# Optimization experiments

Measured on AMD Instinct MI355X. Metric: run time of the kernel, lower is better.

The kernel has to match this reference:

```python
import jax, jax.numpy as jnp
import numpy as np

S, B, HID, NH = 256, 2, 512, 8
HD = HID // NH
C = 1.0            # Poincare ball curvature c (geoopt k = -c)
SQC = C ** 0.5
EPS = 1e-15


def _artanh(x):
    return jnp.arctanh(jnp.clip(x, -1 + 1e-7, 1 - 1e-7))


def artan_k(x):
    return _artanh(SQC * x) / SQC


def tan_k(x):
    return jnp.tanh(SQC * x) / SQC


def mobius_add(x, y):
    x2 = jnp.sum(x * x, -1, keepdims=True)
    y2 = jnp.sum(y * y, -1, keepdims=True)
    xy = jnp.sum(x * y, -1, keepdims=True)
    num = (1 + 2 * C * xy + C * y2) * x + (1 - C * x2) * y
    den = 1 + 2 * C * xy + C * C * x2 * y2
    return num / jnp.maximum(den, EPS)


def mobius_matvec(W, x):
    x_norm = jnp.maximum(jnp.linalg.norm(x, axis=-1, keepdims=True), EPS)
    mx = x @ W.T
    mx_norm = jnp.maximum(jnp.linalg.norm(mx, axis=-1, keepdims=True), EPS)
    res = tan_k(mx_norm / x_norm * artan_k(x_norm)) * (mx / mx_norm)
    zero = jnp.all(mx == 0, axis=-1, keepdims=True)
    return jnp.where(zero, 0.0, res)


def projx(x):
    n = jnp.maximum(jnp.linalg.norm(x, axis=-1, keepdims=True), EPS)
    maxnorm = (1 - 4e-3) / SQC  # float32 eps in geoopt
    return jnp.where(n > maxnorm, x / n * maxnorm, x)


def expmap0(u):
    n = jnp.maximum(jnp.linalg.norm(u, axis=-1, keepdims=True), EPS)
    return tan_k(n) * u / n


def logmap0(y):
    n = jnp.maximum(jnp.linalg.norm(y, axis=-1, keepdims=True), EPS)
    return artan_k(n) * y / n


def mobius_scalar_mul(r, x):
    n = jnp.maximum(jnp.linalg.norm(x, axis=-1, keepdims=True), EPS)
    return tan_k(r * artan_k(n)) * x / n


def manifold_linear(W, b, x):
    return projx(mobius_add(mobius_matvec(W, x), b))


def setup_inputs() -> dict:
    key = jax.random.key(0)
    ks = jax.random.split(key, 7)
    q = jax.random.normal(ks[0], (S, B, HID), jnp.float32) * 0.02
    w = lambda k: jax.random.normal(k, (HID, HID), jnp.float32) * 0.02
    bias = lambda k: jax.random.normal(k, (HID,), jnp.float32) * 0.01
    return {"query": q,
            "Wq": w(ks[1]), "bq": bias(ks[2]),
            "Wk": w(ks[3]), "bk": bias(ks[4]),
            "Wv": w(ks[5]), "bv": bias(ks[6])}


def reference(query, Wq, bq, Wk, bk, Wv, bv):
    x = jnp.transpose(query, (1, 0, 2))  # [B,S,HID], key=value=query
    Bn, Sn, _ = x.shape
    q = manifold_linear(Wq, bq, x)
    k = manifold_linear(Wk, bk, x)
    v = manifold_linear(Wv, bv, x)
    # faithful to torch .view(-1, H, S, D): plain memory reshape (not transpose)
    ql = expmap0(logmap0(q).reshape(Bn, NH, Sn, HD))
    kl = expmap0(logmap0(k).reshape(Bn, NH, Sn, HD))
    vl = expmap0(logmap0(v).reshape(Bn, NH, Sn, HD))
    # pairwise mobius_add(-q, k) -> [B,H,Q,N,D]; torch norm(p=-2) over D (faithful)
    diff = mobius_add(-ql[:, :, :, None, :], kl[:, :, None, :, :])
    t1 = jnp.sum(jnp.maximum(diff * diff, 1e-30) ** -1.0, axis=-1) ** -0.5
    scores = jnp.clip(-2.0 * artan_k(t1), -1e10, 1e10)
    probs = jax.nn.sigmoid(scores)  # [B,H,Q,N]; dropout p=0 -> identity
    # weighted gyro-midpoint over N (geoopt _weighted_midpoint, reducedim=[-1])
    gamma = 2.0 / jnp.maximum(1.0 - C * jnp.sum(vl * vl, -1), EPS)  # [B,H,N]
    denom = jnp.einsum('bhqn,bhn->bhq', probs, gamma - 1.0)
    sgn = jnp.where(denom >= 0, 1.0, -1.0)
    denom = sgn * jnp.maximum(jnp.abs(denom), 1e-10)
    nom = jnp.einsum('bhqn,bhnd->bhqd', probs, gamma[..., None] * vl)
    ctx = mobius_scalar_mul(0.5, nom / denom[..., None])  # [B,H,Q,D]
    ctx = jnp.transpose(ctx, (0, 2, 1, 3))  # [B,Q,H,D]
    ctx = expmap0(logmap0(ctx).reshape(Bn, Sn, HID))
    return jnp.transpose(ctx, (1, 0, 2)), probs
```

## Files before the change

kernel.cpp:

```cpp
#include <hip/hip_runtime.h>
#include <math.h>

constexpr int S_   = 256;
constexpr int B_   = 2;
constexpr int HID_ = 512;
constexpr int NH_  = 8;
constexpr int HD_  = 64;
constexpr int BSH  = B_ * S_ * HID_;

__device__ __forceinline__ float artanh_c(float x) {
    x = fminf(fmaxf(x, -0.9999999f), 0.9999999f);
    return 0.5f * __logf((1.f + x) / (1.f - x));
}

__device__ __forceinline__ float wsum64(float v) {
    #pragma unroll
    for (int o = 1; o < 64; o <<= 1) v += __shfl_xor(v, o, 64);
    return v;
}

__device__ __forceinline__ float block_sum_256(float v, float* red) {
    const int t = threadIdx.x;
    __syncthreads();
    red[t] = v;
    __syncthreads();
    #pragma unroll
    for (int sft = 128; sft > 0; sft >>= 1) {
        if (t < sft) red[t] += red[t + sft];
        __syncthreads();
    }
    return red[0];
}

constexpr int TM_ = 32, TN_ = 64, KC_ = 32;

__global__ __launch_bounds__(256) void gemm3_kernel(
    const float* __restrict__ query,
    const float* __restrict__ Wq, const float* __restrict__ Wk,
    const float* __restrict__ Wv, float* __restrict__ ws_mx)
{
    const int tid   = threadIdx.x;
    const int which = blockIdx.x >> 7;
    const int tmp   = blockIdx.x & 127;
    const int row0  = (tmp >> 3) * TM_;
    const int col0  = (tmp & 7) * TN_;
    const float* __restrict__ W = (which == 0) ? Wq : (which == 1) ? Wk : Wv;
    float* __restrict__ outp = ws_mx + (size_t)which * (HID_ * HID_);

    __shared__ __align__(16) float sA[KC_][68];
    __shared__ __align__(16) float sB[KC_][68];

    const int sr = tid >> 3;
    const int sk = (tid & 7) * 4;
    const int gra = row0 + sr;
    const float* pa  = query + (size_t)((gra & 255) * 2 + (gra >> 8)) * HID_ + sk;
    const float* pb0 = W + (size_t)(col0 + sr) * HID_ + sk;
    const float* pb1 = W + (size_t)(col0 + sr + 32) * HID_ + sk;

    const int ty = tid >> 4, tx = tid & 15;
    float acc[2][4] = {};

    float4 va  = *(const float4*)pa;
    float4 vb0 = *(const float4*)pb0;
    float4 vb1 = *(const float4*)pb1;
    for (int k0 = 0; k0 < HID_; k0 += KC_) {
        __syncthreads();
        sA[sk+0][sr] = va.x;  sA[sk+1][sr] = va.y;  sA[sk+2][sr] = va.z;  sA[sk+3][sr] = va.w;
        sB[sk+0][sr] = vb0.x; sB[sk+1][sr] = vb0.y; sB[sk+2][sr] = vb0.z; sB[sk+3][sr] = vb0.w;
        sB[sk+0][sr+32] = vb1.x; sB[sk+1][sr+32] = vb1.y; sB[sk+2][sr+32] = vb1.z; sB[sk+3][sr+32] = vb1.w;
        __syncthreads();
        if (k0 + KC_ < HID_) {
            va  = *(const float4*)(pa + k0 + KC_);
            vb0 = *(const float4*)(pb0 + k0 + KC_);
            vb1 = *(const float4*)(pb1 + k0 + KC_);
        }
        #pragma unroll
        for (int kk = 0; kk < KC_; ++kk) {
            const float2 av = *(const float2*)&sA[kk][ty * 2];
            const float4 bv = *(const float4*)&sB[kk][tx * 4];
            acc[0][0] = fmaf(av.x, bv.x, acc[0][0]);
            acc[0][1] = fmaf(av.x, bv.y, acc[0][1]);
            acc[0][2] = fmaf(av.x, bv.z, acc[0][2]);
            acc[0][3] = fmaf(av.x, bv.w, acc[0][3]);
            acc[1][0] = fmaf(av.y, bv.x, acc[1][0]);
            acc[1][1] = fmaf(av.y, bv.y, acc[1][1]);
            acc[1][2] = fmaf(av.y, bv.z, acc[1][2]);
            acc[1][3] = fmaf(av.y, bv.w, acc[1][3]);
        }
    }
    #pragma unroll
    for (int i = 0; i < 2; ++i) {
        float4 o = make_float4(acc[i][0], acc[i][1], acc[i][2], acc[i][3]);
        *(float4*)&outp[(size_t)(row0 + ty * 2 + i) * HID_ + col0 + tx * 4] = o;
    }
}

__global__ __launch_bounds__(256) void mobius_rows_kernel(
    const float* __restrict__ query,
    const float* __restrict__ bq, const float* __restrict__ bk,
    const float* __restrict__ bv,
    float* __restrict__ ws_qkv, float* __restrict__ ws_gamma)
{
    const int lane = threadIdx.x & 63;
    const int wv   = threadIdx.x >> 6;
    const int row  = blockIdx.x * 4 + wv;
    const int which = row >> 9;
    const int rr    = row & 511;
    const float* __restrict__ bias = (which == 0) ? bq : (which == 1) ? bk : bv;
    float* mrow = ws_qkv + (size_t)row * HID_;
    const float* xrow = query + (size_t)((rr & 255) * 2 + (rr >> 8)) * HID_;

    float m[8], x[8], bb[8];
    *(float4*)&m[0]  = ((const float4*)mrow)[lane * 2];
    *(float4*)&m[4]  = ((const float4*)mrow)[lane * 2 + 1];
    *(float4*)&x[0]  = ((const float4*)xrow)[lane * 2];
    *(float4*)&x[4]  = ((const float4*)xrow)[lane * 2 + 1];
    *(float4*)&bb[0] = ((const float4*)bias)[lane * 2];
    *(float4*)&bb[4] = ((const float4*)bias)[lane * 2 + 1];

    float x2p = 0.f, m2p = 0.f, b2p = 0.f;
    #pragma unroll
    for (int j = 0; j < 8; ++j) {
        x2p = fmaf(x[j], x[j], x2p);
        m2p = fmaf(m[j], m[j], m2p);
        b2p = fmaf(bb[j], bb[j], b2p);
    }
    const float x2s = wsum64(x2p);
    const float mn2 = wsum64(m2p);
    const float b2s = wsum64(b2p);
    const float xn = fmaxf(sqrtf(x2s), 1e-15f);
    const float mn = fmaxf(sqrtf(mn2), 1e-15f);
    const float fac = tanhf(mn / xn * artanh_c(xn)) / mn;
    float r[8];
    float r2p = 0.f, ryp = 0.f;
    #pragma unroll
    for (int j = 0; j < 8; ++j) {
        r[j] = fac * m[j];
        r2p = fmaf(r[j], r[j], r2p);
        ryp = fmaf(r[j], bb[j], ryp);
    }
    const float r2s = wsum64(r2p);
    const float ry  = wsum64(ryp);
    const float a_c = 1.f + 2.f * ry + b2s;
    const float b_c = 1.f - r2s;
    const float den = 1.f + 2.f * ry + r2s * b2s;
    const float inv_den = 1.f / fmaxf(den, 1e-15f);
    float h[8];
    float h2p = 0.f;
    #pragma unroll
    for (int j = 0; j < 8; ++j) {
        h[j] = (a_c * r[j] + b_c * bb[j]) * inv_den;
        h2p = fmaf(h[j], h[j], h2p);
    }
    const float h2s = wsum64(h2p);
    float hn = fmaxf(sqrtf(h2s), 1e-15f);
    float pf = 1.f;
    if (hn > 0.996f) { pf = 0.996f / hn; hn = 0.996f; }
    const float lf = artanh_c(hn) / hn * pf;
    float l[8];
    float l2p = 0.f;
    #pragma unroll
    for (int j = 0; j < 8; ++j) {
        l[j] = lf * h[j];
        l2p = fmaf(l[j], l[j], l2p);
    }
    float cs = l2p;
    cs += __shfl_xor(cs, 1, 64);
    cs += __shfl_xor(cs, 2, 64);
    cs += __shfl_xor(cs, 4, 64);
    const float cn = fmaxf(sqrtf(cs), 1e-15f);
    const float th = tanhf(cn);
    const float sc = th / cn;
    float o[8];
    #pragma unroll
    for (int j = 0; j < 8; ++j) o[j] = sc * l[j];
    ((float4*)mrow)[lane * 2]     = *(float4*)&o[0];
    ((float4*)mrow)[lane * 2 + 1] = *(float4*)&o[4];
    if (which == 2 && (lane & 7) == 0) {
        const int j = lane >> 3;
        ws_gamma[(size_t)rr * NH_ + j] = 2.f / fmaxf(1.f - th * th, 1e-15f);
    }
}

__global__ __launch_bounds__(256) void attn_kernel(
    const float* __restrict__ ws_qkv, const float* __restrict__ gamma,
    float* __restrict__ probs, float* __restrict__ lc)
{
    const int tid = threadIdx.x;
    const int bh  = blockIdx.x >> 5;
    const int q0  = (blockIdx.x & 31) * 8;
    const float* __restrict__ ql = ws_qkv + (size_t)bh * (S_ * HD_);
    const float* __restrict__ kl = ws_qkv + (size_t)BSH + (size_t)bh * (S_ * HD_);
    const float* __restrict__ vl = ws_qkv + (size_t)2 * BSH + (size_t)bh * (S_ * HD_);

    __shared__ __align__(16) float kS[128 * 64];
    __shared__ __align__(16) float qS[8 * 64];
    __shared__ float pS[8 * 256];
    __shared__ float gS[S_];
    __shared__ float dnS[8];

    gS[tid] = gamma[(size_t)bh * S_ + tid];
    if (tid < 128) ((float4*)qS)[tid] = ((const float4*)(ql + (size_t)q0 * 64))[tid];
    __syncthreads();

    const int q_l = tid >> 5;
    const int n_i = tid & 31;
    float qv[64];
    #pragma unroll
    for (int c = 0; c < 16; ++c)
        *(float4*)&qv[c * 4] = *(const float4*)&qS[q_l * 64 + c * 4];
    float q2 = 0.f;
    #pragma unroll
    for (int d = 0; d < 64; ++d) q2 = fmaf(qv[d], qv[d], q2);
    const float b_c = 1.f - q2;
    float* __restrict__ prow = probs + ((size_t)(bh * S_ + q0 + q_l)) * S_;

    const int c4 = tid & 15;
    const int nb = tid >> 4;
    float sp = 0.f, spg = 0.f;

    for (int half = 0; half < 2; ++half) {
        __syncthreads();
        #pragma unroll
        for (int jj = 0; jj < 8; ++jj) {
            const int n = nb + 16 * jj;
            const float4 v = *(const float4*)(kl + ((size_t)(half * 128 + n)) * 64 + c4 * 4);
            *(float4*)&kS[n * 64 + ((c4 ^ (n & 15)) * 4)] = v;
        }
        __syncthreads();
        #pragma unroll
        for (int j = 0; j < 4; ++j) {
            const int n = n_i + 32 * j;
            float kv[64];
            #pragma unroll
            for (int c = 0; c < 16; ++c)
                *(float4*)&kv[c * 4] = *(const float4*)&kS[n * 64 + ((c ^ (n & 15)) * 4)];
            float s = 0.f, k2 = 0.f;
            #pragma unroll
            for (int d = 0; d < 64; ++d) {
                s  = fmaf(qv[d], kv[d], s);
                k2 = fmaf(kv[d], kv[d], k2);
            }
            const float a_c = 1.f - 2.f * s + k2;
            const float den = fmaxf(fmaf(q2, k2, 1.f - 2.f * s), 1e-15f);
            const float c2  = 1e-30f * den * den;
            float invsum = 0.f;
            #pragma unroll
            for (int d = 0; d < 64; ++d) {
                const float u = fmaf(b_c, kv[d], -(a_c * qv[d]));
                invsum += __builtin_amdgcn_rcpf(fmaf(u, u, c2));
            }
            const float t1 = __builtin_amdgcn_rsqf(den * den * invsum);
            const float p = 0.5f - 0.5f * fminf(t1, 0.9999999f);
            const int gn = half * 128 + n;
            prow[gn] = p;
            const float g = gS[gn];
            pS[q_l * 256 + gn] = p * g;
            sp += p; spg += p * g;
        }
    }
    #pragma unroll
    for (int o = 1; o < 32; o <<= 1) {
        sp  += __shfl_xor(sp, o, 64);
        spg += __shfl_xor(spg, o, 64);
    }
    if ((tid & 31) == 0) dnS[q_l] = spg - sp;
    __syncthreads();

    const int w = tid >> 6, d = tid & 63;
    const float* __restrict__ p0 = &pS[w * 256];
    const float* __restrict__ p1 = &pS[(w + 4) * 256];
    float acc0 = 0.f, acc1 = 0.f;
    #pragma unroll 8
    for (int n = 0; n < 256; ++n) {
        const float v = vl[(size_t)n * 64 + d];
        acc0 = fmaf(p0[n], v, acc0);
        acc1 = fmaf(p1[n], v, acc1);
    }
    #pragma unroll
    for (int t = 0; t < 2; ++t) {
        const int qq = w + 4 * t;
        const float nom = t ? acc1 : acc0;
        const float dd = dnS[qq];
        const float adn = fmaxf(fabsf(dd), 1e-10f);
        const float sden = (dd >= 0.f) ? adn : -adn;
        const float m = nom / sden;
        const float ss = wsum64(m * m);
        const float nn = fmaxf(sqrtf(ss), 1e-15f);
        const float s1 = tanhf(0.5f * artanh_c(nn));
        const float res = s1 * m / nn;
        const float nres = fmaxf(s1, 1e-15f);
        lc[((size_t)(bh * S_ + q0 + qq)) * HD_ + d] = (artanh_c(nres) / nres) * res;
    }
}

__global__ __launch_bounds__(256) void outproj_kernel(
    const float* __restrict__ lc, float* __restrict__ out0)
{
    const int t = threadIdx.x;
    const int s = blockIdx.x & (S_ - 1);
    const int b = blockIdx.x >> 8;
    __shared__ float red[256];
    const int h0 = t >> 6, d0 = t & 63;
    const int e1 = t + 256;
    const int h1 = e1 >> 6, d1 = e1 & 63;
    const float v0 = lc[(((size_t)(b * NH_ + h0)) * S_ + s) * HD_ + d0];
    const float v1 = lc[(((size_t)(b * NH_ + h1)) * S_ + s) * HD_ + d1];
    const float ss = block_sum_256(v0 * v0 + v1 * v1, red);
    const float nn = fmaxf(sqrtf(ss), 1e-15f);
    const float f = tanhf(nn) / nn;
    float* orow = out0 + ((size_t)(s * B_ + b)) * HID_;
    orow[t] = f * v0;
    orow[t + 256] = f * v1;
}

extern "C" void kernel_launch(void* const* d_in, const int* in_sizes, int n_in,
                              void* d_out, int out_size, void* d_ws, size_t ws_size,
                              hipStream_t stream) {
    (void)in_sizes; (void)n_in; (void)out_size; (void)ws_size;
    const float* query = (const float*)d_in[0];
    const float* Wq = (const float*)d_in[1];
    const float* bq = (const float*)d_in[2];
    const float* Wk = (const float*)d_in[3];
    const float* bk = (const float*)d_in[4];
    const float* Wv = (const float*)d_in[5];
    const float* bv = (const float*)d_in[6];

    float* out0  = (float*)d_out;
    float* probs = out0 + (size_t)S_ * B_ * HID_;

    float* ws       = (float*)d_ws;
    float* ws_qkv   = ws;
    float* ws_gamma = ws + (size_t)3 * BSH;
    float* ws_lc    = ws + (size_t)3 * BSH + 4096;

    gemm3_kernel<<<dim3(3 * 128), dim3(256), 0, stream>>>(query, Wq, Wk, Wv, ws_qkv);
    mobius_rows_kernel<<<dim3(384), dim3(256), 0, stream>>>(query, bq, bk, bv, ws_qkv, ws_gamma);
    attn_kernel<<<dim3(512), dim3(256), 0, stream>>>(ws_qkv, ws_gamma, probs, ws_lc);
    outproj_kernel<<<dim3(B_ * S_), dim3(256), 0, stream>>>(ws_lc, out0);
}
```

Before: 130.0 us.

## Shrink GEMM tiles, precompute key norms, rescale inverse-sum, split PV over waves

The projection GEMM now uses 32x32 tiles with 2x2 per-thread outputs, doubling the grid to 768 blocks for better CU fill. In the attention kernel, key squared norms are computed once per key during the shared-memory load via lane shuffles, instead of redundantly per query-key pair. The inner inverse-sum loop is rescaled by 1/a_c so each element needs one fewer multiply. The probs-times-V reduction is split across the four waves by key range and each V element is reused for all eight queries, with partial sums combined through shared memory. Risks include lower per-thread arithmetic intensity in the GEMM, extra shared memory and a barrier, and a small numerical change from dividing by a_c.

```diff
diff --git a/kernel.cpp b/kernel.cpp
--- a/kernel.cpp
+++ b/kernel.cpp
@@ -32,66 +32,56 @@
     return red[0];
 }
 
-constexpr int TM_ = 32, TN_ = 64, KC_ = 32;
-
 __global__ __launch_bounds__(256) void gemm3_kernel(
     const float* __restrict__ query,
     const float* __restrict__ Wq, const float* __restrict__ Wk,
     const float* __restrict__ Wv, float* __restrict__ ws_mx)
 {
     const int tid   = threadIdx.x;
-    const int which = blockIdx.x >> 7;
-    const int tmp   = blockIdx.x & 127;
-    const int row0  = (tmp >> 3) * TM_;
-    const int col0  = (tmp & 7) * TN_;
+    const int which = blockIdx.x >> 8;
+    const int tmp   = blockIdx.x & 255;
+    const int row0  = (tmp >> 4) * 32;
+    const int col0  = (tmp & 15) * 32;
     const float* __restrict__ W = (which == 0) ? Wq : (which == 1) ? Wk : Wv;
     float* __restrict__ outp = ws_mx + (size_t)which * (HID_ * HID_);
 
-    __shared__ __align__(16) float sA[KC_][68];
-    __shared__ __align__(16) float sB[KC_][68];
+    __shared__ __align__(16) float sA[32][36];
+    __shared__ __align__(16) float sB[32][36];
 
     const int sr = tid >> 3;
     const int sk = (tid & 7) * 4;
     const int gra = row0 + sr;
-    const float* pa  = query + (size_t)((gra & 255) * 2 + (gra >> 8)) * HID_ + sk;
-    const float* pb0 = W + (size_t)(col0 + sr) * HID_ + sk;
-    const float* pb1 = W + (size_t)(col0 + sr + 32) * HID_ + sk;
+    const float* pa = query + (size_t)((gra & 255) * 2 + (gra >> 8)) * HID_ + sk;
+    const float* pb = W + (size_t)(col0 + sr) * HID_ + sk;
 
     const int ty = tid >> 4, tx = tid & 15;
-    float acc[2][4] = {};
-
-    float4 va  = *(const float4*)pa;
-    float4 vb0 = *(const float4*)pb0;
-    float4 vb1 = *(const float4*)pb1;
-    for (int k0 = 0; k0 < HID_; k0 += KC_) {
-        __syncthreads();
-        sA[sk+0][sr] = va.x;  sA[sk+1][sr] = va.y;  sA[sk+2][sr] = va.z;  sA[sk+3][sr] = va.w;
-        sB[sk+0][sr] = vb0.x; sB[sk+1][sr] = vb0.y; sB[sk+2][sr] = vb0.z; sB[sk+3][sr] = vb0.w;
-        sB[sk+0][sr+32] = vb1.x; sB[sk+1][sr+32] = vb1.y; sB[sk+2][sr+32] = vb1.z; sB[sk+3][sr+32] = vb1.w;
-        __syncthreads();
-        if (k0 + KC_ < HID_) {
-            va  = *(const float4*)(pa + k0 + KC_);
-            vb0 = *(const float4*)(pb0 + k0 + KC_);
-            vb1 = *(const float4*)(pb1 + k0 + KC_);
-        }
-        #pragma unroll
-        for (int kk = 0; kk < KC_; ++kk) {
+    float acc[2][2] = {};
+
+    float4 va = *(const float4*)pa;
+    float4 vb = *(const float4*)pb;
+    for (int k0 = 0; k0 < HID_; k0 += 32) {
+        __syncthreads();
+        sA[sk+0][sr] = va.x; sA[sk+1][sr] = va.y; sA[sk+2][sr] = va.z; sA[sk+3][sr] = va.w;
+        sB[sk+0][sr] = vb.x; sB[sk+1][sr] = vb.y; sB[sk+2][sr] = vb.z; sB[sk+3][sr] = vb.w;
+        __syncthreads();
+        if (k0 + 32 < HID_) {
+            va = *(const float4*)(pa + k0 + 32);
+            vb = *(const float4*)(pb + k0 + 32);
+        }
+        #pragma unroll
+        for (int kk = 0; kk < 32; ++kk) {
             const float2 av = *(const float2*)&sA[kk][ty * 2];
-            const float4 bv = *(const float4*)&sB[kk][tx * 4];
+            const float2 bv = *(const float2*)&sB[kk][tx * 2];
             acc[0][0] = fmaf(av.x, bv.x, acc[0][0]);
             acc[0][1] = fmaf(av.x, bv.y, acc[0][1]);
-            acc[0][2] = fmaf(av.x, bv.z, acc[0][2]);
-            acc[0][3] = fmaf(av.x, bv.w, acc[0][3]);
             acc[1][0] = fmaf(av.y, bv.x, acc[1][0]);
             acc[1][1] = fmaf(av.y, bv.y, acc[1][1]);
-            acc[1][2] = fmaf(av.y, bv.z, acc[1][2]);
-            acc[1][3] = fmaf(av.y, bv.w, acc[1][3]);
         }
     }
     #pragma unroll
     for (int i = 0; i < 2; ++i) {
-        float4 o = make_float4(acc[i][0], acc[i][1], acc[i][2], acc[i][3]);
-        *(float4*)&outp[(size_t)(row0 + ty * 2 + i) * HID_ + col0 + tx * 4] = o;
+        *(float2*)&outp[(size_t)(row0 + ty * 2 + i) * HID_ + col0 + tx * 2] =
+            make_float2(acc[i][0], acc[i][1]);
     }
 }
 
@@ -195,8 +185,10 @@
 
     __shared__ __align__(16) float kS[128 * 64];
     __shared__ __align__(16) float qS[8 * 64];
-    __shared__ float pS[8 * 256];
+    __shared__ __align__(16) float pS[8 * 256];
     __shared__ float gS[S_];
+    __shared__ float k2S[128];
+    __shared__ float nomP[4][8][64];
     __shared__ float dnS[8];
 
     gS[tid] = gamma[(size_t)bh * S_ + tid];
@@ -226,6 +218,12 @@
             const int n = nb + 16 * jj;
             const float4 v = *(const float4*)(kl + ((size_t)(half * 128 + n)) * 64 + c4 * 4);
             *(float4*)&kS[n * 64 + ((c4 ^ (n & 15)) * 4)] = v;
+            float pk = fmaf(v.x, v.x, fmaf(v.y, v.y, fmaf(v.z, v.z, v.w * v.w)));
+            pk += __shfl_xor(pk, 1, 64);
+            pk += __shfl_xor(pk, 2, 64);
+            pk += __shfl_xor(pk, 4, 64);
+            pk += __shfl_xor(pk, 8, 64);
+            if (c4 == 0) k2S[n] = pk;
         }
         __syncthreads();
         #pragma unroll
@@ -235,22 +233,23 @@
             #pragma unroll
             for (int c = 0; c < 16; ++c)
                 *(float4*)&kv[c * 4] = *(const float4*)&kS[n * 64 + ((c ^ (n & 15)) * 4)];
-            float s = 0.f, k2 = 0.f;
+            float s = 0.f;
             #pragma unroll
-            for (int d = 0; d < 64; ++d) {
-                s  = fmaf(qv[d], kv[d], s);
-                k2 = fmaf(kv[d], kv[d], k2);
-            }
+            for (int d = 0; d < 64; ++d) s = fmaf(qv[d], kv[d], s);
+            const float k2  = k2S[n];
             const float a_c = 1.f - 2.f * s + k2;
             const float den = fmaxf(fmaf(q2, k2, 1.f - 2.f * s), 1e-15f);
-            const float c2  = 1e-30f * den * den;
+            const float ra  = __builtin_amdgcn_rcpf(a_c);
+            const float r_c = b_c * ra;
+            const float scale = den * den * ra * ra;
+            const float c2  = 1e-30f * scale;
             float invsum = 0.f;
             #pragma unroll
             for (int d = 0; d < 64; ++d) {
-                const float u = fmaf(b_c, kv[d], -(a_c * qv[d]));
-                invsum += __builtin_amdgcn_rcpf(fmaf(u, u, c2));
+                const float w = fmaf(r_c, kv[d], -qv[d]);
+                invsum += __builtin_amdgcn_rcpf(fmaf(w, w, c2));
             }
-            const float t1 = __builtin_amdgcn_rsqf(den * den * invsum);
+            const float t1 = __builtin_amdgcn_rsqf(scale * invsum);
             const float p = 0.5f - 0.5f * fminf(t1, 0.9999999f);
             const int gn = half * 128 + n;
             prow[gn] = p;
@@ -268,19 +267,30 @@
     __syncthreads();
 
     const int w = tid >> 6, d = tid & 63;
-    const float* __restrict__ p0 = &pS[w * 256];
-    const float* __restrict__ p1 = &pS[(w + 4) * 256];
-    float acc0 = 0.f, acc1 = 0.f;
-    #pragma unroll 8
-    for (int n = 0; n < 256; ++n) {
-        const float v = vl[(size_t)n * 64 + d];
-        acc0 = fmaf(p0[n], v, acc0);
-        acc1 = fmaf(p1[n], v, acc1);
-    }
+    float acc[8] = {};
+    const float* __restrict__ vbase = vl + (size_t)(w * 64) * 64;
+    #pragma unroll 4
+    for (int i4 = 0; i4 < 16; ++i4) {
+        float vv[4];
+        #pragma unroll
+        for (int j2 = 0; j2 < 4; ++j2) vv[j2] = vbase[(size_t)(i4 * 4 + j2) * 64 + d];
+        #pragma unroll
+        for (int qq = 0; qq < 8; ++qq) {
+            const float4 pq = *(const float4*)&pS[qq * 256 + w * 64 + i4 * 4];
+            acc[qq] = fmaf(pq.x, vv[0], acc[qq]);
+            acc[qq] = fmaf(pq.y, vv[1], acc[qq]);
+            acc[qq] = fmaf(pq.z, vv[2], acc[qq]);
+            acc[qq] = fmaf(pq.w, vv[3], acc[qq]);
+        }
+    }
+    #pragma unroll
+    for (int qq = 0; qq < 8; ++qq) nomP[w][qq][d] = acc[qq];
+    __syncthreads();
+
     #pragma unroll
     for (int t = 0; t < 2; ++t) {
-        const int qq = w + 4 * t;
-        const float nom = t ? acc1 : acc0;
+        const int qq = (tid >> 6) + 4 * t;
+        const float nom = nomP[0][qq][d] + nomP[1][qq][d] + nomP[2][qq][d] + nomP[3][qq][d];
         const float dd = dnS[qq];
         const float adn = fmaxf(fabsf(dd), 1e-10f);
         const float sden = (dd >= 0.f) ? adn : -adn;
@@ -334,7 +344,7 @@
     float* ws_gamma = ws + (size_t)3 * BSH;
     float* ws_lc    = ws + (size_t)3 * BSH + 4096;
 
-    gemm3_kernel<<<dim3(3 * 128), dim3(256), 0, stream>>>(query, Wq, Wk, Wv, ws_qkv);
+    gemm3_kernel<<<dim3(768), dim3(256), 0, stream>>>(query, Wq, Wk, Wv, ws_qkv);
     mobius_rows_kernel<<<dim3(384), dim3(256), 0, stream>>>(query, bq, bk, bv, ws_qkv, ws_gamma);
     attn_kernel<<<dim3(512), dim3(256), 0, stream>>>(ws_qkv, ws_gamma, probs, ws_lc);
     outproj_kernel<<<dim3(B_ * S_), dim3(256), 0, stream>>>(ws_lc, out0);
```

New measurement: 129.3 us. No clear change (-0.5%).
